# Kernel tuning notes

Hardware: AMD Instinct MI355X
Metric: run time of the kernel (lower is better)

The kernel has to match this reference:

```python
import math
import jax, jax.numpy as jnp
import numpy as np

TWO_PI = 2.0 * math.pi
BETA = 1.0
K_COUP = 1.0
A_ANC = 0.08
OMEGA_ANC = TWO_PI * 200.0
B, P, N = 64, 256, 4096


def setup_inputs() -> dict:
    key = jax.random.key(0)
    k1, k2, k3 = jax.random.split(key, 3)
    t = jax.random.uniform(k1, (1,), dtype=jnp.float32)
    phi = jax.random.uniform(k2, (B, N), dtype=jnp.float32) * TWO_PI
    xi = jax.random.uniform(k3, (P, N), dtype=jnp.float32) * TWO_PI
    return {"t": t, "phi": phi, "xi": xi}


def reference(t, phi, xi):
    # diff: (B, P, N)
    diff = phi[:, None, :] - xi[None, :, :]
    m = jnp.cos(diff).sum(-1)                      # (B, P)
    weights = jax.nn.softmax(BETA * m / N, axis=-1)  # (B, P)
    coupling = jnp.einsum('bp,bpn->bn', weights, jnp.sin(diff))  # (B, N)
    dphi = K_COUP * coupling + A_ANC * jnp.sin(OMEGA_ANC * t - phi)
    return dphi
```

## Files before the change

kernel.cpp:

```cpp
#include <hip/hip_runtime.h>
#include <hip/hip_fp16.h>
#include <math.h>

#define B_SZ 64
#define P_SZ 256
#define N_SZ 4096
#define NCA 64
#define A_ANC 0.08f
#define OMEGA_ANC 1256.6370614359172f

typedef _Float16 h2v __attribute__((ext_vector_type(2)));

__device__ __forceinline__ float fdot2f(__half2 a, __half2 b, float c) {
#if __has_builtin(__builtin_amdgcn_fdot2)
    return __builtin_amdgcn_fdot2(__builtin_bit_cast(h2v, a),
                                  __builtin_bit_cast(h2v, b), c, false);
#else
    float2 af = __half22float2(a), bf = __half22float2(b);
    return fmaf(af.x, bf.x, fmaf(af.y, bf.y, c));
#endif
}

__global__ __launch_bounds__(256, 4) void k_mpart_fused(const float* __restrict__ phi,
                                                        const float* __restrict__ xi,
                                                        __half2* __restrict__ XPg,
                                                        float* __restrict__ m_part) {
    const int pt = blockIdx.x;
    const int nc = blockIdx.y;
    const int tid = threadIdx.x;
    const int b = tid & 63;
    const int g = tid >> 6;

    __shared__ __half2 xs[64][20];
    __shared__ __half2 ps[64][66];

    const int p0 = pt * 16, n0 = nc * 64;

#pragma unroll
    for (int k = 0; k < 4; ++k) {
        int idx = tid + k * 256;
        int p_l = idx >> 6, n_l = idx & 63;
        float s, c;
        __sincosf(xi[(p0 + p_l) * N_SZ + n0 + n_l], &s, &c);
        __half2 h = __floats2half2_rn(c, s);
        xs[n_l][p_l] = h;
        XPg[(p0 + p_l) * N_SZ + n0 + n_l] = h;
    }
#pragma unroll 4
    for (int k = 0; k < 16; ++k) {
        int idx = tid + k * 256;
        int bb = idx >> 6, n_l = idx & 63;
        float s, c;
        __sincosf(phi[bb * N_SZ + n0 + n_l], &s, &c);
        ps[n_l][bb] = __floats2half2_rn(c, s);
    }
    __syncthreads();

    float4 acc = {0.f, 0.f, 0.f, 0.f};
#pragma unroll 8
    for (int n_l = 0; n_l < 64; ++n_l) {
        __half2 pp = ps[n_l][b];
        const __half2* row = &xs[n_l][g * 4];
        acc.x = fdot2f(row[0], pp, acc.x);
        acc.y = fdot2f(row[1], pp, acc.y);
        acc.z = fdot2f(row[2], pp, acc.z);
        acc.w = fdot2f(row[3], pp, acc.w);
    }
    *(float4*)&m_part[(nc * 64 + b) * 256 + p0 + 4 * g] = acc;
}

__global__ __launch_bounds__(256) void k_weights(const float* __restrict__ m_part,
                                                 float* __restrict__ weights) {
    const int b = blockIdx.x;
    const int tid = threadIdx.x;
    const int wv = tid >> 6;
    __shared__ float sred[8];

    float msum = 0.f;
#pragma unroll 8
    for (int c = 0; c < NCA; ++c)
        msum += m_part[(c * 64 + b) * 256 + tid];
    float logit = msum * (1.0f / 4096.0f);

    float v = logit;
    for (int o = 32; o > 0; o >>= 1) v = fmaxf(v, __shfl_xor(v, o));
    if ((tid & 63) == 0) sred[wv] = v;
    __syncthreads();
    float mx = fmaxf(fmaxf(sred[0], sred[1]), fmaxf(sred[2], sred[3]));
    float e = __expf(logit - mx);
    v = e;
    for (int o = 32; o > 0; o >>= 1) v += __shfl_xor(v, o);
    if ((tid & 63) == 0) sred[4 + wv] = v;
    __syncthreads();
    float s = sred[4] + sred[5] + sred[6] + sred[7];
    weights[b * 256 + tid] = e / s;
}

__global__ __launch_bounds__(256, 2) void k_coupling(const __half2* __restrict__ XP,
                                                     const float* __restrict__ weights,
                                                     const float* __restrict__ phi,
                                                     const float* __restrict__ t_ptr,
                                                     float* __restrict__ out) {
    const int bt = blockIdx.x;
    const int nc = blockIdx.y;
    const int tid = threadIdx.x;
    const int b_l = tid >> 6;
    const int lane = tid & 63;

    __shared__ float wsh[4][256];
    for (int idx = tid; idx < 4 * 256; idx += 256) {
        int bb = idx >> 8, p = idx & 255;
        wsh[bb][p] = weights[(bt * 4 + bb) * 256 + p];
    }
    __syncthreads();

    const int n = nc * 128 + 2 * lane;
    const __half2* col = XP + n;
    float aC0 = 0.f, aS0 = 0.f, aC1 = 0.f, aS1 = 0.f;

#pragma unroll 2
    for (int p = 0; p < 256; p += 4) {
        float4 w4 = *(const float4*)&wsh[b_l][p];
        const float w[4] = {w4.x, w4.y, w4.z, w4.w};
#pragma unroll
        for (int k = 0; k < 4; ++k) {
            uint2 v = *(const uint2*)&col[(p + k) * N_SZ];
            __half2 h0 = __builtin_bit_cast(__half2, v.x);
            __half2 h1 = __builtin_bit_cast(__half2, v.y);
            aC0 = fmaf(w[k], __low2float(h0), aC0);
            aS0 = fmaf(w[k], __high2float(h0), aS0);
            aC1 = fmaf(w[k], __low2float(h1), aC1);
            aS1 = fmaf(w[k], __high2float(h1), aS1);
        }
    }

    const int b = bt * 4 + b_l;
    const float wt = OMEGA_ANC * t_ptr[0];
    float2 ph2 = *(const float2*)&phi[b * N_SZ + n];
    float s0, c0, s1, c1;
    __sincosf(ph2.x, &s0, &c0);
    __sincosf(ph2.y, &s1, &c1);
    float2 o;
    o.x = fmaf(A_ANC, __sinf(wt - ph2.x), s0 * aC0 - c0 * aS0);
    o.y = fmaf(A_ANC, __sinf(wt - ph2.y), s1 * aC1 - c1 * aS1);
    *(float2*)&out[b * N_SZ + n] = o;
}

extern "C" void kernel_launch(void* const* d_in, const int* in_sizes, int n_in,
                              void* d_out, int out_size, void* d_ws, size_t ws_size,
                              hipStream_t stream) {
    const float* t   = (const float*)d_in[0];
    const float* phi = (const float*)d_in[1];
    const float* xi  = (const float*)d_in[2];
    float* out = (float*)d_out;

    char* w = (char*)d_ws;
    __half2* XP    = (__half2*)w;
    float* m_part  = (float*)(w + 4u * 1024 * 1024);
    float* weights = (float*)(w + 8u * 1024 * 1024);

    k_mpart_fused<<<dim3(16, NCA), 256, 0, stream>>>(phi, xi, XP, m_part);
    k_weights<<<64, 256, 0, stream>>>(m_part, weights);
    k_coupling<<<dim3(16, 32), 256, 0, stream>>>(XP, weights, phi, t, out);
}
```

Baseline: 90.02 us.

## Compute m-partials with MFMA, split xi sincos kernel, widen coupling loads

Moves the xi sin/cos table into its own elementwise kernel and recomputes the B×P partial dot products with 16x16x32 f16 MFMA instructions, reading phi directly and computing sincos per fragment instead of going through LDS. The number of N-chunk partials is halved. The coupling kernel now handles four n per lane using 128-bit loads, with half as many blocks. In exchange this adds a kernel launch, recomputes phi sincos redundantly across P tiles, and lowers occupancy in the coupling kernel.

```diff
diff --git a/kernel.cpp b/kernel.cpp
--- a/kernel.cpp
+++ b/kernel.cpp
@@ -5,68 +5,55 @@
 #define B_SZ 64
 #define P_SZ 256
 #define N_SZ 4096
-#define NCA 64
+#define NCA 32
 #define A_ANC 0.08f
 #define OMEGA_ANC 1256.6370614359172f
 
-typedef _Float16 h2v __attribute__((ext_vector_type(2)));
+typedef _Float16 half8 __attribute__((ext_vector_type(8)));
+typedef float floatx4 __attribute__((ext_vector_type(4)));
 
-__device__ __forceinline__ float fdot2f(__half2 a, __half2 b, float c) {
-#if __has_builtin(__builtin_amdgcn_fdot2)
-    return __builtin_amdgcn_fdot2(__builtin_bit_cast(h2v, a),
-                                  __builtin_bit_cast(h2v, b), c, false);
-#else
-    float2 af = __half22float2(a), bf = __half22float2(b);
-    return fmaf(af.x, bf.x, fmaf(af.y, bf.y, c));
-#endif
+__global__ __launch_bounds__(256) void k_xp(const float* __restrict__ xi,
+                                            __half2* __restrict__ XP) {
+    int idx = blockIdx.x * 256 + threadIdx.x;
+    float s, c;
+    __sincosf(xi[idx], &s, &c);
+    XP[idx] = __floats2half2_rn(c, s);
 }
 
-__global__ __launch_bounds__(256, 4) void k_mpart_fused(const float* __restrict__ phi,
-                                                        const float* __restrict__ xi,
-                                                        __half2* __restrict__ XPg,
-                                                        float* __restrict__ m_part) {
-    const int pt = blockIdx.x;
-    const int nc = blockIdx.y;
-    const int tid = threadIdx.x;
-    const int b = tid & 63;
-    const int g = tid >> 6;
+__global__ __launch_bounds__(256) void k_mpart_mfma(const float* __restrict__ phi,
+                                                    const __half2* __restrict__ XP,
+                                                    float* __restrict__ m_part) {
+    const int bt = blockIdx.x & 3;
+    const int pt = blockIdx.x >> 2;
+    const int w  = threadIdx.x >> 6;
+    const int lane = threadIdx.x & 63;
+    const int m = lane & 15;
+    const int q = lane >> 4;
 
-    __shared__ __half2 xs[64][20];
-    __shared__ __half2 ps[64][66];
+    const int c  = blockIdx.y * 4 + w;
+    const int n0 = c * 128;
+    const int b_row = bt * 16 + m;
+    const int p_row = pt * 16 + m;
 
-    const int p0 = pt * 16, n0 = nc * 64;
-
+    floatx4 acc = {0.f, 0.f, 0.f, 0.f};
 #pragma unroll
-    for (int k = 0; k < 4; ++k) {
-        int idx = tid + k * 256;
-        int p_l = idx >> 6, n_l = idx & 63;
-        float s, c;
-        __sincosf(xi[(p0 + p_l) * N_SZ + n0 + n_l], &s, &c);
-        __half2 h = __floats2half2_rn(c, s);
-        xs[n_l][p_l] = h;
-        XPg[(p0 + p_l) * N_SZ + n0 + n_l] = h;
+    for (int s = 0; s < 8; ++s) {
+        const int nb = n0 + s * 16 + q * 4;
+        float4 ph = *(const float4*)&phi[b_row * N_SZ + nb];
+        half8 bf = *(const half8*)&XP[p_row * N_SZ + nb];
+        half8 af;
+        float ss, cc;
+        __sincosf(ph.x, &ss, &cc); af[0] = (_Float16)cc; af[1] = (_Float16)ss;
+        __sincosf(ph.y, &ss, &cc); af[2] = (_Float16)cc; af[3] = (_Float16)ss;
+        __sincosf(ph.z, &ss, &cc); af[4] = (_Float16)cc; af[5] = (_Float16)ss;
+        __sincosf(ph.w, &ss, &cc); af[6] = (_Float16)cc; af[7] = (_Float16)ss;
+        acc = __builtin_amdgcn_mfma_f32_16x16x32_f16(af, bf, acc, 0, 0, 0);
     }
-#pragma unroll 4
-    for (int k = 0; k < 16; ++k) {
-        int idx = tid + k * 256;
-        int bb = idx >> 6, n_l = idx & 63;
-        float s, c;
-        __sincosf(phi[bb * N_SZ + n0 + n_l], &s, &c);
-        ps[n_l][bb] = __floats2half2_rn(c, s);
+#pragma unroll
+    for (int r = 0; r < 4; ++r) {
+        int b = bt * 16 + q * 4 + r;
+        m_part[(c * 64 + b) * 256 + pt * 16 + m] = acc[r];
     }
-    __syncthreads();
-
-    float4 acc = {0.f, 0.f, 0.f, 0.f};
-#pragma unroll 8
-    for (int n_l = 0; n_l < 64; ++n_l) {
-        __half2 pp = ps[n_l][b];
-        const __half2* row = &xs[n_l][g * 4];
-        acc.x = fdot2f(row[0], pp, acc.x);
-        acc.y = fdot2f(row[1], pp, acc.y);
-        acc.z = fdot2f(row[2], pp, acc.z);
-        acc.w = fdot2f(row[3], pp, acc.w);
-    }
-    *(float4*)&m_part[(nc * 64 + b) * 256 + p0 + 4 * g] = acc;
 }
 
 __global__ __launch_bounds__(256) void k_weights(const float* __restrict__ m_part,
@@ -96,15 +83,15 @@
     weights[b * 256 + tid] = e / s;
 }
 
-__global__ __launch_bounds__(256, 2) void k_coupling(const __half2* __restrict__ XP,
-                                                     const float* __restrict__ weights,
-                                                     const float* __restrict__ phi,
-                                                     const float* __restrict__ t_ptr,
-                                                     float* __restrict__ out) {
+__global__ __launch_bounds__(256) void k_coupling(const __half2* __restrict__ XP,
+                                                  const float* __restrict__ weights,
+                                                  const float* __restrict__ phi,
+                                                  const float* __restrict__ t_ptr,
+                                                  float* __restrict__ out) {
     const int bt = blockIdx.x;
     const int nc = blockIdx.y;
     const int tid = threadIdx.x;
-    const int b_l = tid >> 6;
+    const int w = tid >> 6;
     const int lane = tid & 63;
 
     __shared__ float wsh[4][256];
@@ -114,36 +101,39 @@
     }
     __syncthreads();
 
-    const int n = nc * 128 + 2 * lane;
+    const int n = nc * 256 + lane * 4;
     const __half2* col = XP + n;
     float aC0 = 0.f, aS0 = 0.f, aC1 = 0.f, aS1 = 0.f;
+    float aC2 = 0.f, aS2 = 0.f, aC3 = 0.f, aS3 = 0.f;
 
-#pragma unroll 2
-    for (int p = 0; p < 256; p += 4) {
-        float4 w4 = *(const float4*)&wsh[b_l][p];
-        const float w[4] = {w4.x, w4.y, w4.z, w4.w};
-#pragma unroll
-        for (int k = 0; k < 4; ++k) {
-            uint2 v = *(const uint2*)&col[(p + k) * N_SZ];
-            __half2 h0 = __builtin_bit_cast(__half2, v.x);
-            __half2 h1 = __builtin_bit_cast(__half2, v.y);
-            aC0 = fmaf(w[k], __low2float(h0), aC0);
-            aS0 = fmaf(w[k], __high2float(h0), aS0);
-            aC1 = fmaf(w[k], __low2float(h1), aC1);
-            aS1 = fmaf(w[k], __high2float(h1), aS1);
-        }
+#pragma unroll 16
+    for (int p = 0; p < 256; ++p) {
+        uint4 v = *(const uint4*)&col[p * N_SZ];
+        float wgt = wsh[w][p];
+        __half2 h0 = __builtin_bit_cast(__half2, v.x);
+        __half2 h1 = __builtin_bit_cast(__half2, v.y);
+        __half2 h2 = __builtin_bit_cast(__half2, v.z);
+        __half2 h3 = __builtin_bit_cast(__half2, v.w);
+        aC0 = fmaf(wgt, __low2float(h0), aC0); aS0 = fmaf(wgt, __high2float(h0), aS0);
+        aC1 = fmaf(wgt, __low2float(h1), aC1); aS1 = fmaf(wgt, __high2float(h1), aS1);
+        aC2 = fmaf(wgt, __low2float(h2), aC2); aS2 = fmaf(wgt, __high2float(h2), aS2);
+        aC3 = fmaf(wgt, __low2float(h3), aC3); aS3 = fmaf(wgt, __high2float(h3), aS3);
     }
 
-    const int b = bt * 4 + b_l;
+    const int b = bt * 4 + w;
     const float wt = OMEGA_ANC * t_ptr[0];
-    float2 ph2 = *(const float2*)&phi[b * N_SZ + n];
-    float s0, c0, s1, c1;
-    __sincosf(ph2.x, &s0, &c0);
-    __sincosf(ph2.y, &s1, &c1);
-    float2 o;
-    o.x = fmaf(A_ANC, __sinf(wt - ph2.x), s0 * aC0 - c0 * aS0);
-    o.y = fmaf(A_ANC, __sinf(wt - ph2.y), s1 * aC1 - c1 * aS1);
-    *(float2*)&out[b * N_SZ + n] = o;
+    float4 ph4 = *(const float4*)&phi[b * N_SZ + n];
+    float s0, c0, s1, c1, s2, c2, s3, c3;
+    __sincosf(ph4.x, &s0, &c0);
+    __sincosf(ph4.y, &s1, &c1);
+    __sincosf(ph4.z, &s2, &c2);
+    __sincosf(ph4.w, &s3, &c3);
+    float4 o;
+    o.x = fmaf(A_ANC, __sinf(wt - ph4.x), s0 * aC0 - c0 * aS0);
+    o.y = fmaf(A_ANC, __sinf(wt - ph4.y), s1 * aC1 - c1 * aS1);
+    o.z = fmaf(A_ANC, __sinf(wt - ph4.z), s2 * aC2 - c2 * aS2);
+    o.w = fmaf(A_ANC, __sinf(wt - ph4.w), s3 * aC3 - c3 * aS3);
+    *(float4*)&out[b * N_SZ + n] = o;
 }
 
 extern "C" void kernel_launch(void* const* d_in, const int* in_sizes, int n_in,
@@ -157,9 +147,10 @@
     char* w = (char*)d_ws;
     __half2* XP    = (__half2*)w;
     float* m_part  = (float*)(w + 4u * 1024 * 1024);
-    float* weights = (float*)(w + 8u * 1024 * 1024);
+    float* weights = (float*)(w + 6u * 1024 * 1024);
 
-    k_mpart_fused<<<dim3(16, NCA), 256, 0, stream>>>(phi, xi, XP, m_part);
+    k_xp<<<(P_SZ * N_SZ) / 256, 256, 0, stream>>>(xi, XP);
+    k_mpart_mfma<<<dim3(64, 8), 256, 0, stream>>>(phi, XP, m_part);
     k_weights<<<64, 256, 0, stream>>>(m_part, weights);
-    k_coupling<<<dim3(16, 32), 256, 0, stream>>>(XP, weights, phi, t, out);
+    k_coupling<<<dim3(16, 16), 256, 0, stream>>>(XP, weights, phi, t, out);
 }
```

Measured after the change: 135.2 us. +50.2%, slower.
